# Performance work log

Hardware: AMD Instinct MI355X
Metric: run time of the kernel (lower is better)

## Reference

```python
import jax, jax.numpy as jnp
import numpy as np

B, N, D, H = 4, 2048, 64, 8

def setup_inputs() -> dict:
    key = jax.random.key(0)
    ks = jax.random.split(key, 6)
    s = 0.05
    return {
        "x":  jax.random.normal(ks[0], (B, N, D), dtype=jnp.float32),
        "Wq": jax.random.normal(ks[1], (D, D * H), dtype=jnp.float32) * s,
        "Wk": jax.random.normal(ks[2], (D, D * H), dtype=jnp.float32) * s,
        "Wv": jax.random.normal(ks[3], (D, D * H), dtype=jnp.float32) * s,
        "Wu": jax.random.normal(ks[4], (D * H, D), dtype=jnp.float32) * s,
        "bu": jnp.zeros((D,), dtype=jnp.float32),
    }

def reference(x, Wq, Wk, Wv, Wu, bu):
    b, n, d = x.shape
    h = Wq.shape[1] // d
    # projections: each head has full width d (per the original module)
    q = (x @ Wq).reshape(b, n, h, d).transpose(0, 2, 1, 3)  # [b,h,n,d]
    k = (x @ Wk).reshape(b, n, h, d).transpose(0, 2, 1, 3)
    v = (x @ Wv).reshape(b, n, h, d).transpose(0, 2, 1, 3)
    scores = jnp.einsum('bhnd,bhmd->bhnm', q, k) / jnp.sqrt(jnp.float32(d))
    w = jax.nn.softmax(scores, axis=-1)
    y = jnp.einsum('bhnm,bhmd->bhnd', w, v)          # [b,h,n,d]
    y = y.transpose(0, 2, 1, 3).reshape(b, n, h * d)  # [b,n,h*d]
    return y @ Wu + bu
```

## Files before the change

### kernel.cpp

```cpp
#include <hip/hip_runtime.h>
#include <hip/hip_bf16.h>

#define BB 4
#define NN 2048
#define DD 64
#define HH 8
#define DHH 512

typedef __bf16 bf16_t;
typedef __bf16 bf16x8 __attribute__((ext_vector_type(8)));
typedef __bf16 bf16x4 __attribute__((ext_vector_type(4)));
typedef float f32x4 __attribute__((ext_vector_type(4)));
typedef long long i64;
typedef i64 i64x2 __attribute__((ext_vector_type(2)));
typedef _Float16 f16_t;
typedef _Float16 f16x4 __attribute__((ext_vector_type(4)));
typedef __fp16 h16x2 __attribute__((ext_vector_type(2)));

__device__ __forceinline__ void dma16(const void* g, void* l) {
    __builtin_amdgcn_global_load_lds(
        (const __attribute__((address_space(1))) unsigned int*)g,
        (__attribute__((address_space(3))) unsigned int*)l,
        16, 0, 0);
}

#define MFMA   __builtin_amdgcn_mfma_f32_16x16x32_bf16
#define MFMA8  __builtin_amdgcn_mfma_f32_16x16x32_fp8_fp8
#define MFMA16F __builtin_amdgcn_mfma_f32_16x16x16f16

#define QSCALE 0.18033688011112042f


__global__ __launch_bounds__(256) void prep(
    const float* __restrict__ Wq, const float* __restrict__ Wk,
    const float* __restrict__ Wv, const float* __restrict__ Wu,
    bf16_t* __restrict__ Wqt, bf16_t* __restrict__ Wkt,
    bf16_t* __restrict__ Wvt, bf16_t* __restrict__ Wut)
{
    const int bid = blockIdx.x, tid = threadIdx.x;
    if (bid < 12) {
        const int m = bid >> 2, slice = bid & 3;
        const float* src = (m == 0) ? Wq : (m == 1) ? Wk : Wv;
        bf16_t* dst = (m == 0) ? Wqt : (m == 1) ? Wkt : Wvt;
        const float scale = (m == 0) ? QSCALE : 1.0f;
        const int dc = slice * 128 + (tid >> 1);
        const int kbase = (tid & 1) * 32;
        #pragma unroll
        for (int k0 = 0; k0 < 4; ++k0) {
            bf16x8 p;
            #pragma unroll
            for (int j = 0; j < 8; ++j)
                p[j] = (bf16_t)(src[(size_t)(kbase + k0 * 8 + j) * 512 + dc] * scale);
            *(bf16x8*)(dst + dc * 64 + kbase + k0 * 8) = p;
        }
    } else {
        const int kq = (bid - 12) * 128;
        const int dc = tid >> 2, sub = (tid & 3) * 32;
        #pragma unroll
        for (int k0 = 0; k0 < 4; ++k0) {
            bf16x8 p;
            #pragma unroll
            for (int j = 0; j < 8; ++j)
                p[j] = (bf16_t)Wu[(size_t)(kq + sub + k0 * 8 + j) * 64 + dc];
            *(bf16x8*)(Wut + dc * 512 + kq + sub + k0 * 8) = p;
        }
    }
}

__global__ __launch_bounds__(256) void qkv_mfma(
    const float* __restrict__ x, const bf16_t* __restrict__ Wqt,
    const bf16_t* __restrict__ Wkt, const bf16_t* __restrict__ Wvt,
    char* __restrict__ q8, char* __restrict__ k8, f16_t* __restrict__ vt)
{
    const int n0   = blockIdx.x * 64;
    const int h    = blockIdx.y;
    const int tid  = threadIdx.x;
    const int w    = tid >> 6;
    const int lane = tid & 63;
    const int quad = lane >> 4;
    const int c    = lane & 15;
    const int cq   = c & 7;
    const int l8   = lane >> 3;
    const int lg   = (lane & 7) ^ l8;
    const int lo   = l8 * 128 + lg * 16;
    const int sw0  = ((quad    ) ^ cq) * 16;
    const int sw1  = ((quad + 4) ^ cq) * 16;
    const int w2048 = w * 2048;

    __shared__ __align__(16) float  xs[64 * 64];
    __shared__ __align__(16) bf16_t Wqs[64 * 64], Wks[64 * 64], Wvs[64 * 64];

    {
        const int rloc = lane >> 4;
        const int s    = lane & 15;
        #pragma unroll
        for (int j = 0; j < 4; ++j) {
            int chunk = w * 4 + j;
            int r7 = (chunk * 4 + rloc) & 7;
            const char* src = (const char*)(x + (size_t)(n0 + chunk * 4 + rloc) * 64)
                            + ((s & 8) | ((s & 7) ^ r7)) * 16;
            dma16(src, (char*)xs + chunk * 1024);
        }
    }
    const char* qg = (const char*)Wqt + (size_t)h * 8192;
    const char* kg = (const char*)Wkt + (size_t)h * 8192;
    const char* vg = (const char*)Wvt + (size_t)h * 8192;
    dma16(qg + w2048 + lo,        (char*)Wqs + w2048);
    dma16(qg + w2048 + 1024 + lo, (char*)Wqs + w2048 + 1024);
    dma16(kg + w2048 + lo,        (char*)Wks + w2048);
    dma16(kg + w2048 + 1024 + lo, (char*)Wks + w2048 + 1024);
    dma16(vg + w2048 + lo,        (char*)Wvs + w2048);
    dma16(vg + w2048 + 1024 + lo, (char*)Wvs + w2048 + 1024);
    __syncthreads();

    auto xfrag = [&](int row, int kk) -> bf16x8 {
        const char* rbase = (const char*)xs + row * 256;
        int g0 = kk * 8 + ((quad * 2    ) ^ cq);
        int g1 = kk * 8 + ((quad * 2 + 1) ^ cq);
        f32x4 a = *(const f32x4*)(rbase + g0 * 16);
        f32x4 b = *(const f32x4*)(rbase + g1 * 16);
        bf16x8 r;
        r[0] = (bf16_t)a[0]; r[1] = (bf16_t)a[1]; r[2] = (bf16_t)a[2]; r[3] = (bf16_t)a[3];
        r[4] = (bf16_t)b[0]; r[5] = (bf16_t)b[1]; r[6] = (bf16_t)b[2]; r[7] = (bf16_t)b[3];
        return r;
    };

    bf16x8 xf0 = xfrag(w * 16 + c, 0);
    bf16x8 xf1 = xfrag(w * 16 + c, 1);

    const int gr = n0 + w * 16 + c;
    const int bb = gr >> 11, nn = gr & 2047;
    char* qrow_g = q8 + (((size_t)bb * HH + h) * NN + nn) * 64;
    char* krow_g = k8 + (((size_t)bb * HH + h) * NN + nn) * 64;
    const int nsw = (nn & 3) ^ ((nn >> 2) & 3);

    #pragma unroll
    for (int mb = 0; mb < 4; ++mb) {
        const char* aq = (const char*)Wqs + (mb * 16 + c) * 128;
        const char* ak = (const char*)Wks + (mb * 16 + c) * 128;
        f32x4 accq = (f32x4){0.f, 0.f, 0.f, 0.f};
        f32x4 acck = (f32x4){0.f, 0.f, 0.f, 0.f};
        accq = MFMA(*(const bf16x8*)(aq + sw0), xf0, accq, 0, 0, 0);
        accq = MFMA(*(const bf16x8*)(aq + sw1), xf1, accq, 0, 0, 0);
        acck = MFMA(*(const bf16x8*)(ak + sw0), xf0, acck, 0, 0, 0);
        acck = MFMA(*(const bf16x8*)(ak + sw1), xf1, acck, 0, 0, 0);
        int g2  = (mb * 2 + (quad >> 1)) & 3;
        int off = ((quad & 1) * 4) + ((mb >> 1) * 8) + ((g2 ^ nsw) * 16);
        int pq = __builtin_amdgcn_cvt_pk_fp8_f32(accq[0], accq[1], 0, false);
        pq     = __builtin_amdgcn_cvt_pk_fp8_f32(accq[2], accq[3], pq, true);
        int pk = __builtin_amdgcn_cvt_pk_fp8_f32(acck[0], acck[1], 0, false);
        pk     = __builtin_amdgcn_cvt_pk_fp8_f32(acck[2], acck[3], pk, true);
        *(int*)(qrow_g + off) = pq;
        *(int*)(krow_g + off) = pk;
    }

    const char* wvrow = (const char*)Wvs + (w * 16 + c) * 128;
    bf16x8 vf0 = *(const bf16x8*)(wvrow + sw0);
    bf16x8 vf1 = *(const bf16x8*)(wvrow + sw1);

    const int bb2 = n0 >> 11;
    f16_t* vtb = vt + ((size_t)bb2 * HH + h) * (size_t)(DD * NN)
               + (size_t)((n0 & 2047) >> 4) * 1024 + quad * 256 + (w * 16 + c) * 4;

    #pragma unroll
    for (int nb = 0; nb < 4; ++nb) {
        f32x4 acc = (f32x4){0.f, 0.f, 0.f, 0.f};
        acc = MFMA(xfrag(nb * 16 + c, 0), vf0, acc, 0, 0, 0);
        acc = MFMA(xfrag(nb * 16 + c, 1), vf1, acc, 0, 0, 0);
        f16x4 p = { (f16_t)acc[0], (f16_t)acc[1], (f16_t)acc[2], (f16_t)acc[3] };
        *(f16x4*)(vtb + nb * 1024) = p;
    }
}

__global__ __launch_bounds__(256, 3) void flash_attn(
    const char* __restrict__ q8, const char* __restrict__ k8,
    const f16_t* __restrict__ vt, bf16_t* __restrict__ y)
{
    const int h    = blockIdx.x;
    const int n0   = blockIdx.y * 64;
    const int b    = blockIdx.z;
    const int tid  = threadIdx.x;
    const int w    = tid >> 6;
    const int lane = tid & 63;
    const int quad = lane >> 4;
    const int c    = lane & 15;
    const int ksw  = (quad ^ (c & 3) ^ ((c >> 2) & 3)) * 16;

    __shared__ __align__(16) char SM[49152];

    const size_t bh = (size_t)(b * HH + h);
    const char* qp = q8 + bh * (size_t)(NN * 64);
    const char* kp = k8 + bh * (size_t)(NN * 64);
    const char* vp = (const char*)(vt + bh * (size_t)(DD * NN));

    i64x2 qf[4];
    #pragma unroll
    for (int cb = 0; cb < 4; ++cb)
        qf[cb] = *(const i64x2*)(qp + (size_t)(n0 + cb * 16 + c) * 64 + ksw);

    const char* kdma = kp + w * 1024 + lane * 16;
    const char* vdma = vp + w * 2048 + lane * 16;

    const int kro = w * 2048 + c * 64 + ksw;
    const int vro = 8192 + w * 4096 + quad * 512 + c * 8;

    f32x4 lsum4[4];
    f32x4 o[4][4];
    #pragma unroll
    for (int cb = 0; cb < 4; ++cb) lsum4[cb] = (f32x4){0.f, 0.f, 0.f, 0.f};
    #pragma unroll
    for (int db = 0; db < 4; ++db)
        #pragma unroll
        for (int cb = 0; cb < 4; ++cb) o[db][cb] = (f32x4){0.f, 0.f, 0.f, 0.f};

    #define STAGE2(p, buf) do {                                               \
        char* B_ = SM + (buf) * 24576;                                        \
        const size_t t0_ = (size_t)(2 * (p));                                 \
        dma16(kdma + t0_ * 4096,         B_ + w * 2048);                      \
        dma16(kdma + t0_ * 4096 + 4096,  B_ + w * 2048 + 1024);               \
        dma16(vdma + t0_ * 8192,         B_ + 8192 + w * 4096);               \
        dma16(vdma + t0_ * 8192 + 1024,  B_ + 8192 + w * 4096 + 1024);        \
        dma16(vdma + t0_ * 8192 + 8192,  B_ + 8192 + w * 4096 + 2048);        \
        dma16(vdma + t0_ * 8192 + 9216,  B_ + 8192 + w * 4096 + 3072);        \
    } while (0)

    #define BODY2(buf, hf) do {                                               \
        const char* kb_b = SM + (buf) * 24576;                                \
        i64x2 kf_ = *(const i64x2*)(kb_b + kro + (hf) * 1024);                \
        f16x4 vf_[4];                                                         \
        _Pragma("unroll")                                                     \
        for (int db = 0; db < 4; ++db)                                        \
            vf_[db] = *(const f16x4*)(kb_b + vro + (hf) * 2048 + db * 128);   \
        _Pragma("unroll")                                                     \
        for (int cb = 0; cb < 4; ++cb) {                                      \
            f32x4 s_ = (f32x4){0.f, 0.f, 0.f, 0.f};                           \
            s_ = MFMA8(kf_.x, qf[cb].x, s_, 0, 0, 0);                         \
            s_ = MFMA8(kf_.y, qf[cb].y, s_, 0, 0, 0);                         \
            float p0_ = __builtin_amdgcn_exp2f(s_[0]);                        \
            float p1_ = __builtin_amdgcn_exp2f(s_[1]);                        \
            float p2_ = __builtin_amdgcn_exp2f(s_[2]);                        \
            float p3_ = __builtin_amdgcn_exp2f(s_[3]);                        \
            lsum4[cb] += (f32x4){p0_, p1_, p2_, p3_};                         \
            h16x2 ab_ = __builtin_amdgcn_cvt_pkrtz(p0_, p1_);                 \
            h16x2 cd_ = __builtin_amdgcn_cvt_pkrtz(p2_, p3_);                 \
            f16x4 pf_;                                                        \
            __builtin_memcpy(&pf_, &ab_, 4);                                  \
            __builtin_memcpy((char*)&pf_ + 4, &cd_, 4);                       \
            _Pragma("unroll")                                                 \
            for (int db = 0; db < 4; ++db)                                    \
                o[db][cb] = MFMA16F(vf_[db], pf_, o[db][cb], 0, 0, 0);        \
        }                                                                     \
    } while (0)

    STAGE2(0, 0);
    __syncthreads();
    STAGE2(1, 1);

    #pragma unroll 1
    for (int p = 0; p < 16; ++p) {
        if (p > 0) {
            __syncthreads();
            if (p < 15) STAGE2(p + 1, (p + 1) & 1);
        }
        BODY2(p & 1, 0);
        BODY2(p & 1, 1);
    }

    #undef STAGE2
    #undef BODY2

    float lsum[4];
    #pragma unroll
    for (int cb = 0; cb < 4; ++cb)
        lsum[cb] = (lsum4[cb][0] + lsum4[cb][1]) + (lsum4[cb][2] + lsum4[cb][3]);

    __syncthreads();

    char*  Ob = SM;
    float* Lb = (float*)(SM + 16384);

    #pragma unroll
    for (int cb = 0; cb < 4; ++cb) {
        lsum[cb] += __shfl_xor(lsum[cb], 16, 64);
        lsum[cb] += __shfl_xor(lsum[cb], 32, 64);
    }
    if (quad == 0) {
        #pragma unroll
        for (int cb = 0; cb < 4; ++cb)
            Lb[(w * 4 + cb) * 16 + c] = lsum[cb];
    }

    #pragma unroll
    for (int ww = 0; ww < 4; ++ww) {
        if (w == ww) {
            #pragma unroll
            for (int db = 0; db < 4; ++db) {
                #pragma unroll
                for (int cb = 0; cb < 4; ++cb) {
                    char* p = Ob + (size_t)(((db * 4 + cb) * 4 + quad) * 16 + c) * 16;
                    f32x4 v = o[db][cb];
                    if (ww > 0) v += *(const f32x4*)p;
                    *(f32x4*)p = v;
                }
            }
        }
        __syncthreads();
    }

    {
        const int n_loc = tid & 63;
        const int dq    = tid >> 6;
        const int qcb   = n_loc >> 4;
        const int cc    = n_loc & 15;
        float l = Lb[(0 * 4 + qcb) * 16 + cc] + Lb[(1 * 4 + qcb) * 16 + cc]
                + Lb[(2 * 4 + qcb) * 16 + cc] + Lb[(3 * 4 + qcb) * 16 + cc];
        float inv = 1.0f / l;
        float vals[16];
        #pragma unroll
        for (int q2 = 0; q2 < 4; ++q2) {
            f32x4 v = *(const f32x4*)(Ob
                    + (size_t)(((dq * 4 + qcb) * 4 + q2) * 16 + cc) * 16);
            vals[q2 * 4 + 0] = v[0]; vals[q2 * 4 + 1] = v[1];
            vals[q2 * 4 + 2] = v[2]; vals[q2 * 4 + 3] = v[3];
        }
        bf16x8 o0, o1;
        #pragma unroll
        for (int j = 0; j < 8; ++j) {
            o0[j] = (bf16_t)(vals[j] * inv);
            o1[j] = (bf16_t)(vals[8 + j] * inv);
        }
        bf16_t* yrow = y + bh * (size_t)(NN * DD) + (size_t)(n0 + n_loc) * DD + dq * 16;
        *(bf16x8*)(yrow)     = o0;
        *(bf16x8*)(yrow + 8) = o1;
    }
}

__global__ __launch_bounds__(256) void out_proj(
    const bf16_t* __restrict__ y,
    const bf16_t* __restrict__ Wut,
    const float* __restrict__ bu, float* __restrict__ out)
{
    const int rt   = blockIdx.x >> 1;
    const int dh   = blockIdx.x & 1;
    const int row0 = rt * 32;
    const int b    = row0 >> 11;
    const int nn0  = row0 & 2047;
    const int tid  = threadIdx.x;
    const int w    = tid >> 6;
    const int lane = tid & 63;
    const int quad = lane >> 4;
    const int c    = lane & 15;
    const int cq   = c & 7;

    __shared__ __align__(16) bf16_t ys[32 * 512];

    {
        const int hsel = lane >> 3;
        const int g7   = lane & 7;
        #pragma unroll
        for (int rr = 0; rr < 8; ++rr) {
            int row = w * 8 + rr;
            const char* src = (const char*)y
                + (((size_t)b * HH + hsel) * NN + nn0 + row) * 128
                + ((g7 ^ (row & 7)) * 16);
            dma16(src, (char*)ys + row * 1024);
        }
    }
    __syncthreads();

    const int rows16 = (w >> 1) * 16;
    const int mb     = dh * 2 + (w & 1);
    const char* yrow = (const char*)ys + (rows16 + c) * 1024;

    f32x4 acc = (f32x4){0.f, 0.f, 0.f, 0.f};
    #pragma unroll
    for (int kk = 0; kk < 16; ++kk) {
        int g = kk * 4 + quad;
        bf16x8 bfrag = *(const bf16x8*)(yrow + (((g & ~7) | ((g & 7) ^ cq)) * 16));
        bf16x8 afrag = *(const bf16x8*)((const char*)Wut
                        + (size_t)(mb * 16 + c) * 1024 + kk * 64 + quad * 16);
        acc = MFMA(afrag, bfrag, acc, 0, 0, 0);
    }

    float4 bb = *(const float4*)(bu + mb * 16 + quad * 4);
    float4 res = { acc[0] + bb.x, acc[1] + bb.y, acc[2] + bb.z, acc[3] + bb.w };
    float* op = out + (size_t)(row0 + rows16 + c) * DD + mb * 16 + quad * 4;
    *(float4*)op = res;
}

extern "C" void kernel_launch(void* const* d_in, const int* in_sizes, int n_in,
                              void* d_out, int out_size, void* d_ws, size_t ws_size,
                              hipStream_t stream) {
    const float* x  = (const float*)d_in[0];
    const float* Wq = (const float*)d_in[1];
    const float* Wk = (const float*)d_in[2];
    const float* Wv = (const float*)d_in[3];
    const float* Wu = (const float*)d_in[4];
    const float* bu = (const float*)d_in[5];
    float* out = (float*)d_out;

    const size_t SEG8 = (size_t)BB * HH * NN * 64;
    const size_t SEG  = SEG8 * 2;
    char* ws = (char*)d_ws;
    char*   q8  = ws;
    char*   k8  = ws + SEG8;
    f16_t*  vt  = (f16_t*)(ws + 2 * SEG8);
    bf16_t* y   = (bf16_t*)(ws + 2 * SEG8 + SEG);
    bf16_t* Wqt = (bf16_t*)(ws + 2 * SEG8 + 2 * SEG);
    bf16_t* Wkt = (bf16_t*)(ws + 2 * SEG8 + 2 * SEG + (1 << 16));
    bf16_t* Wvt = (bf16_t*)(ws + 2 * SEG8 + 2 * SEG + 2 * (1 << 16));
    bf16_t* Wut = (bf16_t*)(ws + 2 * SEG8 + 2 * SEG + 3 * (1 << 16));

    prep<<<dim3(16), dim3(256), 0, stream>>>(Wq, Wk, Wv, Wu, Wqt, Wkt, Wvt, Wut);
    qkv_mfma<<<dim3(128, 8), dim3(256), 0, stream>>>(x, Wqt, Wkt, Wvt, q8, k8, vt);
    flash_attn<<<dim3(HH, NN / 64, BB), dim3(256), 0, stream>>>(q8, k8, vt, y);
    out_proj<<<dim3(512), dim3(256), 0, stream>>>(y, Wut, bu, out);
}
```

Before: 128.1 us.

## Share K/V LDS tiles across two query groups with 512-thread attention blocks

Flash attention blocks now handle 128 queries with 8 waves: two query groups of four waves each, sharing the same double-buffered K/V LDS tiles. DMA staging is split between the two groups, so each K/V tile is loaded once per 128 queries instead of once per 64. This halves K/V global traffic and staging per query. In exchange the block is larger, the grid has half as many blocks, more threads wait at each barrier, and the launch bound now allows four 512-thread blocks, which may limit registers.

```diff
diff --git a/kernel.cpp b/kernel.cpp
--- a/kernel.cpp
+++ b/kernel.cpp
@@ -172,15 +172,17 @@
     }
 }
 
-__global__ __launch_bounds__(256, 3) void flash_attn(
+__global__ __launch_bounds__(512, 4) void flash_attn(
     const char* __restrict__ q8, const char* __restrict__ k8,
     const f16_t* __restrict__ vt, bf16_t* __restrict__ y)
 {
     const int h    = blockIdx.x;
-    const int n0   = blockIdx.y * 64;
+    const int nb0  = blockIdx.y * 128;
     const int b    = blockIdx.z;
     const int tid  = threadIdx.x;
     const int w    = tid >> 6;
+    const int wq   = w >> 2;
+    const int wk   = w & 3;
     const int lane = tid & 63;
     const int quad = lane >> 4;
     const int c    = lane & 15;
@@ -193,16 +195,17 @@
     const char* kp = k8 + bh * (size_t)(NN * 64);
     const char* vp = (const char*)(vt + bh * (size_t)(DD * NN));
 
+    const int qbase = nb0 + wq * 64;
     i64x2 qf[4];
     #pragma unroll
     for (int cb = 0; cb < 4; ++cb)
-        qf[cb] = *(const i64x2*)(qp + (size_t)(n0 + cb * 16 + c) * 64 + ksw);
-
-    const char* kdma = kp + w * 1024 + lane * 16;
-    const char* vdma = vp + w * 2048 + lane * 16;
-
-    const int kro = w * 2048 + c * 64 + ksw;
-    const int vro = 8192 + w * 4096 + quad * 512 + c * 8;
+        qf[cb] = *(const i64x2*)(qp + (size_t)(qbase + cb * 16 + c) * 64 + ksw);
+
+    const char* kdma = kp + wk * 1024 + lane * 16;
+    const char* vdma = vp + wk * 2048 + lane * 16;
+
+    const int kro = wk * 2048 + c * 64 + ksw;
+    const int vro = 8192 + wk * 4096 + quad * 512 + c * 8;
 
     f32x4 lsum4[4];
     f32x4 o[4][4];
@@ -216,12 +219,15 @@
     #define STAGE2(p, buf) do {                                               \
         char* B_ = SM + (buf) * 24576;                                        \
         const size_t t0_ = (size_t)(2 * (p));                                 \
-        dma16(kdma + t0_ * 4096,         B_ + w * 2048);                      \
-        dma16(kdma + t0_ * 4096 + 4096,  B_ + w * 2048 + 1024);               \
-        dma16(vdma + t0_ * 8192,         B_ + 8192 + w * 4096);               \
-        dma16(vdma + t0_ * 8192 + 1024,  B_ + 8192 + w * 4096 + 1024);        \
-        dma16(vdma + t0_ * 8192 + 8192,  B_ + 8192 + w * 4096 + 2048);        \
-        dma16(vdma + t0_ * 8192 + 9216,  B_ + 8192 + w * 4096 + 3072);        \
+        if (wq == 0) {                                                        \
+            dma16(kdma + t0_ * 4096,         B_ + wk * 2048);                 \
+            dma16(kdma + t0_ * 4096 + 4096,  B_ + wk * 2048 + 1024);          \
+            dma16(vdma + t0_ * 8192,         B_ + 8192 + wk * 4096);          \
+        } else {                                                              \
+            dma16(vdma + t0_ * 8192 + 1024,  B_ + 8192 + wk * 4096 + 1024);   \
+            dma16(vdma + t0_ * 8192 + 8192,  B_ + 8192 + wk * 4096 + 2048);   \
+            dma16(vdma + t0_ * 8192 + 9216,  B_ + 8192 + wk * 4096 + 3072);   \
+        }                                                                     \
     } while (0)
 
     #define BODY2(buf, hf) do {                                               \
@@ -276,8 +282,8 @@
 
     __syncthreads();
 
-    char*  Ob = SM;
-    float* Lb = (float*)(SM + 16384);
+    char*  Obh = SM + wq * 16384;
+    float* Lbh = (float*)(SM + 32768 + wq * 1024);
 
     #pragma unroll
     for (int cb = 0; cb < 4; ++cb) {
@@ -287,17 +293,17 @@
     if (quad == 0) {
         #pragma unroll
         for (int cb = 0; cb < 4; ++cb)
-            Lb[(w * 4 + cb) * 16 + c] = lsum[cb];
+            Lbh[(wk * 4 + cb) * 16 + c] = lsum[cb];
     }
 
     #pragma unroll
     for (int ww = 0; ww < 4; ++ww) {
-        if (w == ww) {
+        if (wk == ww) {
             #pragma unroll
             for (int db = 0; db < 4; ++db) {
                 #pragma unroll
                 for (int cb = 0; cb < 4; ++cb) {
-                    char* p = Ob + (size_t)(((db * 4 + cb) * 4 + quad) * 16 + c) * 16;
+                    char* p = Obh + (size_t)(((db * 4 + cb) * 4 + quad) * 16 + c) * 16;
                     f32x4 v = o[db][cb];
                     if (ww > 0) v += *(const f32x4*)p;
                     *(f32x4*)p = v;
@@ -308,17 +314,21 @@
     }
 
     {
-        const int n_loc = tid & 63;
-        const int dq    = tid >> 6;
-        const int qcb   = n_loc >> 4;
-        const int cc    = n_loc & 15;
-        float l = Lb[(0 * 4 + qcb) * 16 + cc] + Lb[(1 * 4 + qcb) * 16 + cc]
-                + Lb[(2 * 4 + qcb) * 16 + cc] + Lb[(3 * 4 + qcb) * 16 + cc];
+        const int n_loc = tid & 127;
+        const int dq    = tid >> 7;
+        const int qh    = n_loc >> 6;
+        const int r64   = n_loc & 63;
+        const int qcb   = r64 >> 4;
+        const int cc    = r64 & 15;
+        const char*  Or = SM + qh * 16384;
+        const float* Lr = (const float*)(SM + 32768 + qh * 1024);
+        float l = Lr[(0 * 4 + qcb) * 16 + cc] + Lr[(1 * 4 + qcb) * 16 + cc]
+                + Lr[(2 * 4 + qcb) * 16 + cc] + Lr[(3 * 4 + qcb) * 16 + cc];
         float inv = 1.0f / l;
         float vals[16];
         #pragma unroll
         for (int q2 = 0; q2 < 4; ++q2) {
-            f32x4 v = *(const f32x4*)(Ob
+            f32x4 v = *(const f32x4*)(Or
                     + (size_t)(((dq * 4 + qcb) * 4 + q2) * 16 + cc) * 16);
             vals[q2 * 4 + 0] = v[0]; vals[q2 * 4 + 1] = v[1];
             vals[q2 * 4 + 2] = v[2]; vals[q2 * 4 + 3] = v[3];
@@ -329,7 +339,8 @@
             o0[j] = (bf16_t)(vals[j] * inv);
             o1[j] = (bf16_t)(vals[8 + j] * inv);
         }
-        bf16_t* yrow = y + bh * (size_t)(NN * DD) + (size_t)(n0 + n_loc) * DD + dq * 16;
+        bf16_t* yrow = y + bh * (size_t)(NN * DD)
+                     + (size_t)(nb0 + n_loc) * DD + dq * 16;
         *(bf16x8*)(yrow)     = o0;
         *(bf16x8*)(yrow + 8) = o1;
     }
@@ -413,6 +424,6 @@
 
     prep<<<dim3(16), dim3(256), 0, stream>>>(Wq, Wk, Wv, Wu, Wqt, Wkt, Wvt, Wut);
     qkv_mfma<<<dim3(128, 8), dim3(256), 0, stream>>>(x, Wqt, Wkt, Wvt, q8, k8, vt);
-    flash_attn<<<dim3(HH, NN / 64, BB), dim3(256), 0, stream>>>(q8, k8, vt, y);
+    flash_attn<<<dim3(HH, NN / 128, BB), dim3(512), 0, stream>>>(q8, k8, vt, y);
     out_proj<<<dim3(512), dim3(256), 0, stream>>>(y, Wut, bu, out);
 }
```

Result: no change. 128.0 us (-0.1%).
